# Optimization experiments

Measured on AMD Instinct MI355X. Metric: run time of the kernel, lower is better.

Reference implementation:

```python
import jax, jax.numpy as jnp
import numpy as np

EPS_COS = 1e-8   # torch F.cosine_similarity norm clamp
EPS_LN = 1e-5    # torch LayerNorm eps


def setup_inputs() -> dict:
    key = jax.random.key(0)
    ks = jax.random.split(key, 8)
    B, P, T, D, H = 512, 200000, 4, 64, 256
    return {
        "target_feat": jax.random.normal(ks[0], (B, D), jnp.float32),
        "source_protos": jax.random.normal(ks[1], (P, T, D), jnp.float32),
        "W1": jax.random.normal(ks[2], (3 * D, H), jnp.float32) * 0.05,
        "b1": jnp.zeros((H,), jnp.float32),
        "ln_g": jnp.ones((H,), jnp.float32),
        "ln_b": jnp.zeros((H,), jnp.float32),
        "W2": jax.random.normal(ks[3], (H, H), jnp.float32) * 0.05,
        "b2": jnp.zeros((H,), jnp.float32),
        "W3": jax.random.normal(ks[4], (H, D), jnp.float32) * 0.05,
        "b3": jnp.zeros((D,), jnp.float32),
        "top_k": 3,
    }


def _layernorm(x, g, b):
    mu = jnp.mean(x, axis=-1, keepdims=True)
    var = jnp.mean(jnp.square(x - mu), axis=-1, keepdims=True)
    return (x - mu) * jax.lax.rsqrt(var + EPS_LN) * g + b


def reference(target_feat, source_protos, W1, b1, ln_g, ln_b, W2, b2, W3, b3, top_k):
    # --- retrieve_similar_prototypes (batched over B queries) ---
    centers = jnp.mean(source_protos, axis=1)              # [P, D]
    tn = target_feat / jnp.maximum(
        jnp.linalg.norm(target_feat, axis=-1, keepdims=True), EPS_COS)
    cn = centers / jnp.maximum(
        jnp.linalg.norm(centers, axis=-1, keepdims=True), EPS_COS)
    sims = jnp.einsum("bd,pd->bp", tn, cn)                 # [B, P] cosine sims
    top_vals, top_idx = jax.lax.top_k(sims, top_k)         # [B, K]
    similar_protos = centers[top_idx]                      # [B, K, D] gather

    # --- interpolate_new_prototype ---
    weights = jax.nn.softmax(top_vals, axis=-1)            # [B, K]
    weighted = jnp.einsum("bkd,bk->bd", similar_protos, weights)
    concat = jnp.concatenate(
        [weighted, similar_protos[:, 0], target_feat], axis=-1)  # [B, 3D]

    h = jax.nn.relu(_layernorm(concat @ W1 + b1, ln_g, ln_b))
    h = jax.nn.relu(h @ W2 + b2)
    new_proto = h @ W3 + b3                                # [B, D]
    return new_proto
```

## Files before the change

### kernel.cpp

```cpp
#include <hip/hip_runtime.h>

#define PTOT 200000
#define NB 512
#define DD 64
#define PT 256
#define NBLK ((PTOT + PT - 1) / PT)
#define NPAD (NBLK * PT)
#define NP3 (NBLK * 3)
#define NCAND 8

typedef __attribute__((ext_vector_type(4))) float f32x4;
typedef __attribute__((ext_vector_type(8))) __bf16 bf16x8;

__device__ __forceinline__ ushort f2bf(float f){
  uint u = __float_as_uint(f);
  u += 0x7FFFu + ((u >> 16) & 1u);
  return (ushort)(u >> 16);
}

__device__ __forceinline__ void ins3(uint& k0, uint& k1, uint& k2, uint key){
  uint t0 = k0 > key ? k0 : key;
  uint m0 = k0 > key ? key : k0;
  uint t1 = k1 > m0 ? k1 : m0;
  uint m1 = k1 > m0 ? m0 : k1;
  k2 = k2 > m1 ? k2 : m1;
  k1 = t1; k0 = t0;
}

__global__ __launch_bounds__(256) void kA_stream(const float* __restrict__ sp,
                                                 const float* __restrict__ tf,
                                                 ushort* __restrict__ cn,
                                                 float* __restrict__ tnf,
                                                 ushort* __restrict__ tnb){
  const int gid = blockIdx.x * 256 + threadIdx.x;
  const int row = gid >> 2;
  const int q = gid & 3;
  const bool istgt = row >= NPAD;

  f32x4 v[4][4];
  if (!istgt){
    if (row < PTOT){
      const float* base = sp + (size_t)row * 256 + q * 16;
      #pragma unroll
      for (int t = 0; t < 4; ++t){
        #pragma unroll
        for (int j = 0; j < 4; ++j)
          v[t][j] = *(const f32x4*)(base + t * 64 + j * 4);
      }
    } else {
      #pragma unroll
      for (int t = 0; t < 4; ++t)
        #pragma unroll
        for (int j = 0; j < 4; ++j)
          v[t][j] = (f32x4){0.f, 0.f, 0.f, 0.f};
    }
  } else {
    const float* base = tf + (size_t)(row - NPAD) * 64 + q * 16;
    #pragma unroll
    for (int j = 0; j < 4; ++j){
      v[0][j] = *(const f32x4*)(base + j * 4);
      v[1][j] = v[0][j]; v[2][j] = v[0][j]; v[3][j] = v[0][j];
    }
  }

  f32x4 c[4];
  float ss = 0.f;
  #pragma unroll
  for (int j = 0; j < 4; ++j){
    c[j] = ((v[0][j] + v[1][j]) + (v[2][j] + v[3][j])) * 0.25f;
    ss += c[j].x*c[j].x + c[j].y*c[j].y + c[j].z*c[j].z + c[j].w*c[j].w;
  }
  ss += __shfl_xor(ss, 1, 64);
  ss += __shfl_xor(ss, 2, 64);
  float rn = 1.0f / fmaxf(sqrtf(ss), 1e-8f);

  uint u[8];
  #pragma unroll
  for (int j = 0; j < 4; ++j){
    u[2*j]   = (uint)f2bf(c[j].x * rn) | ((uint)f2bf(c[j].y * rn) << 16);
    u[2*j+1] = (uint)f2bf(c[j].z * rn) | ((uint)f2bf(c[j].w * rn) << 16);
  }
  if (!istgt){
    uint4* dst = (uint4*)(cn + (size_t)row * 64 + q * 16);
    dst[0] = make_uint4(u[0], u[1], u[2], u[3]);
    dst[1] = make_uint4(u[4], u[5], u[6], u[7]);
  } else {
    const int b = row - NPAD;
    float* fd = tnf + (size_t)b * 64 + q * 16;
    #pragma unroll
    for (int j = 0; j < 4; ++j)
      *(f32x4*)(fd + j * 4) = c[j] * rn;
    uint4* hd = (uint4*)(tnb + (size_t)b * 64 + q * 16);
    hd[0] = make_uint4(u[0], u[1], u[2], u[3]);
    hd[1] = make_uint4(u[4], u[5], u[6], u[7]);
  }
}

__global__ __launch_bounds__(256, 4) void kB_scan(const ushort* __restrict__ cn,
                                                  const ushort* __restrict__ tnb,
                                                  uint* __restrict__ cand){
  __shared__ __align__(16) ushort lds[PT * 64];
  const int tid = threadIdx.x;
  const int blk = blockIdx.x;
  const int wave = tid >> 6;
  const int lane = tid & 63;
  const int l15 = lane & 15;
  const int lg  = lane >> 4;

  {
    const char* src = (const char*)(cn + (size_t)blk * PT * 64);
    #pragma unroll
    for (int k = 0; k < 8; ++k){
      int off = (k * 256 + tid) * 16;
      f32x4 v = *(const f32x4*)(src + off);
      int dst = off ^ (((off >> 7) & 7) << 4);
      *(f32x4*)((char*)lds + dst) = v;
    }
  }
  __syncthreads();

  #pragma unroll 2
  for (int bt8 = 0; bt8 < 8; ++bt8){
    const int bt = wave * 8 + bt8;
    const ushort* tp = tnb + (size_t)(bt * 16 + l15) * 64 + lg * 8;
    bf16x8 bf0 = *(const bf16x8*)(tp);
    bf16x8 bf1 = *(const bf16x8*)(tp + 32);
    uint k0 = 0, k1 = 0, k2 = 0;
    #pragma unroll 4
    for (int ps = 0; ps < 16; ++ps){
      const int p = ps * 16 + l15;
      const int base = p * 128;
      const int sw = (p & 7) << 4;
      bf16x8 a0 = *(const bf16x8*)((const char*)lds + ((base + lg * 16) ^ sw));
      bf16x8 a1 = *(const bf16x8*)((const char*)lds + ((base + 64 + lg * 16) ^ sw));
      f32x4 z = {0.f, 0.f, 0.f, 0.f};
      f32x4 acc = __builtin_amdgcn_mfma_f32_16x16x32_bf16(a0, bf0, z, 0, 0, 0);
      acc = __builtin_amdgcn_mfma_f32_16x16x32_bf16(a1, bf1, acc, 0, 0, 0);
      #pragma unroll
      for (int j = 0; j < 4; ++j){
        uint key = (__float_as_uint(fmaxf(acc[j], 0.0f)) & 0xFFFFFE00u)
                 | (uint)(ps * 16 + lg * 4 + j);
        ins3(k0, k1, k2, key);
      }
    }
    #pragma unroll
    for (int m = 16; m <= 32; m <<= 1){
      uint o0 = (uint)__shfl_xor((int)k0, m, 64);
      uint o1 = (uint)__shfl_xor((int)k1, m, 64);
      uint o2 = (uint)__shfl_xor((int)k2, m, 64);
      ins3(k0, k1, k2, o0); ins3(k0, k1, k2, o1); ins3(k0, k1, k2, o2);
    }
    if (lane < 16){
      int b = bt * 16 + l15;
      uint* dst = cand + ((size_t)blk * NB + b) * 3;
      dst[0] = k0; dst[1] = k1; dst[2] = k2;
    }
  }
}

__global__ __launch_bounds__(256) void kC_fuse(const uint* __restrict__ cand,
    const float* __restrict__ sp, const float* __restrict__ tnf,
    const float* __restrict__ tf,
    const float* __restrict__ W1, const float* __restrict__ b1,
    const float* __restrict__ lng, const float* __restrict__ lnb,
    const float* __restrict__ W2, const float* __restrict__ b2,
    const float* __restrict__ W3, const float* __restrict__ b3,
    float* __restrict__ out){
  __shared__ float cc[4][192];
  __shared__ float h1[4][256];
  __shared__ float h2[4][256];
  const int tid = threadIdx.x;
  const int lane = tid & 63;
  const int w = tid >> 6;
  const int rb = blockIdx.x * 4;
  const int b = rb + w;

  uint k0 = 0, k1 = 0, k2 = 0; int j0 = 0, j1 = 0, j2 = 0;
  for (int i = 0; i < (NP3 + 63) / 64; ++i){
    int j = lane + i * 64;
    uint k = 0;
    if (j < NP3){
      int t = j / 3, r = j - t * 3;
      k = cand[(size_t)t * (NB * 3) + b * 3 + r];
    }
    if (k > k0){ k2=k1; j2=j1; k1=k0; j1=j0; k0=k; j0=j; }
    else if (k > k1){ k2=k1; j2=j1; k1=k; j1=j; }
    else if (k > k2){ k2=k; j2=j; }
  }
  int pcand[NCAND];
  #pragma unroll
  for (int it = 0; it < NCAND; ++it){
    uint wk = k0; int wj = j0;
    #pragma unroll
    for (int m = 1; m < 64; m <<= 1){
      uint ok = (uint)__shfl_xor((int)wk, m, 64);
      int  oj = __shfl_xor(wj, m, 64);
      if (ok > wk || (ok == wk && oj > wj)){ wk = ok; wj = oj; }
    }
    pcand[it] = min((wj / 3) * PT + (int)(wk & 0x1FFu), PTOT - 1);
    if (k0 == wk && j0 == wj){ k0=k1; j0=j1; k1=k2; j1=j2; k2=0; j2=0; }
  }
  float xc[NCAND], es[NCAND];
  const float tno = tnf[b * 64 + lane];
  #pragma unroll
  for (int c = 0; c < NCAND; ++c){
    const float* base = sp + (size_t)pcand[c] * 256 + lane;
    float x = 0.25f * (base[0] + base[64] + base[128] + base[192]);
    float ss = x * x;
    float dt = x * tno;
    #pragma unroll
    for (int m = 1; m < 64; m <<= 1){
      ss += __shfl_xor(ss, m, 64);
      dt += __shfl_xor(dt, m, 64);
    }
    xc[c] = x;
    es[c] = dt / fmaxf(sqrtf(ss), 1e-8f);
  }
  float v0 = -3.0e38f, v1 = v0, v2 = v0;
  int s0 = 0, s1 = 0, s2 = 0;
  #pragma unroll
  for (int c = 0; c < NCAND; ++c){
    float v = es[c];
    if (v > v0){ v2=v1; s2=s1; v1=v0; s1=s0; v0=v; s0=c; }
    else if (v > v1){ v2=v1; s2=s1; v1=v; s1=c; }
    else if (v > v2){ v2=v; s2=c; }
  }
  float e1 = expf(v1 - v0), e2 = expf(v2 - v0);
  float inv = 1.0f / (1.0f + e1 + e2);
  float w0 = inv, w1 = e1 * inv, w2 = e2 * inv;
  float wsum = 0.f, ctop = 0.f;
  #pragma unroll
  for (int c = 0; c < NCAND; ++c){
    float coef = (c == s0) ? w0 : (c == s1) ? w1 : (c == s2) ? w2 : 0.f;
    wsum = fmaf(xc[c], coef, wsum);
    ctop += (c == s0) ? xc[c] : 0.f;
  }
  cc[w][lane]       = wsum;
  cc[w][64 + lane]  = ctop;
  cc[w][128 + lane] = tf[b * 64 + lane];
  __syncthreads();

  {
    const int h = tid;
    float a0 = b1[h]; float a1 = a0, a2 = a0, a3 = a0;
    for (int k = 0; k < 192; ++k){
      float wv = W1[k * 256 + h];
      a0 = fmaf(cc[0][k], wv, a0);
      a1 = fmaf(cc[1][k], wv, a1);
      a2 = fmaf(cc[2][k], wv, a2);
      a3 = fmaf(cc[3][k], wv, a3);
    }
    h1[0][h] = a0; h1[1][h] = a1; h1[2][h] = a2; h1[3][h] = a3;
  }
  __syncthreads();
  {
    float v[4]; float s = 0.f, q = 0.f;
    #pragma unroll
    for (int j = 0; j < 4; ++j){
      v[j] = h1[w][lane + 64 * j];
      s += v[j]; q += v[j] * v[j];
    }
    #pragma unroll
    for (int m = 1; m < 64; m <<= 1){
      s += __shfl_xor(s, m, 64);
      q += __shfl_xor(q, m, 64);
    }
    float mu = s * (1.0f / 256.0f);
    float var = q * (1.0f / 256.0f) - mu * mu;
    float rs = rsqrtf(var + 1e-5f);
    #pragma unroll
    for (int j = 0; j < 4; ++j){
      int hh = lane + 64 * j;
      float y = (v[j] - mu) * rs * lng[hh] + lnb[hh];
      h1[w][hh] = fmaxf(y, 0.0f);
    }
  }
  __syncthreads();
  {
    const int h = tid;
    float a0 = b2[h]; float a1 = a0, a2 = a0, a3 = a0;
    for (int k = 0; k < 256; ++k){
      float wv = W2[k * 256 + h];
      a0 = fmaf(h1[0][k], wv, a0);
      a1 = fmaf(h1[1][k], wv, a1);
      a2 = fmaf(h1[2][k], wv, a2);
      a3 = fmaf(h1[3][k], wv, a3);
    }
    h2[0][h] = fmaxf(a0, 0.f); h2[1][h] = fmaxf(a1, 0.f);
    h2[2][h] = fmaxf(a2, 0.f); h2[3][h] = fmaxf(a3, 0.f);
  }
  __syncthreads();
  {
    const int d = tid & 63, q = tid >> 6;
    float a = b3[d];
    for (int k = 0; k < 256; ++k)
      a = fmaf(h2[q][k], W3[k * 64 + d], a);
    out[(size_t)(rb + q) * 64 + d] = a;
  }
}

extern "C" void kernel_launch(void* const* d_in, const int* in_sizes, int n_in,
                              void* d_out, int out_size, void* d_ws, size_t ws_size,
                              hipStream_t stream){
  const float* tf = (const float*)d_in[0];
  const float* sp = (const float*)d_in[1];
  const float* W1 = (const float*)d_in[2];
  const float* b1 = (const float*)d_in[3];
  const float* lng = (const float*)d_in[4];
  const float* lnb = (const float*)d_in[5];
  const float* W2 = (const float*)d_in[6];
  const float* b2 = (const float*)d_in[7];
  const float* W3 = (const float*)d_in[8];
  const float* b3 = (const float*)d_in[9];
  float* out = (float*)d_out;

  char* ws = (char*)d_ws;
  const size_t off_tnb  = 0;
  const size_t off_tnf  = 65536;
  const size_t off_cn   = 65536 + 131072;
  const size_t cn_bytes = (size_t)NPAD * 64 * 2;
  const size_t off_cand = off_cn + cn_bytes;
  const size_t need = off_cand + (size_t)NBLK * NB * 3 * 4;
  if (ws_size < need) return;

  ushort* tnb = (ushort*)(ws + off_tnb);
  float*  tnf = (float*)(ws + off_tnf);
  ushort* cnb = (ushort*)(ws + off_cn);
  uint*   cand = (uint*)(ws + off_cand);

  const int nthreads = (NPAD + NB) * 4;
  kA_stream<<<nthreads / 256, 256, 0, stream>>>(sp, tf, cnb, tnf, tnb);
  kB_scan<<<NBLK, 256, 0, stream>>>(cnb, tnb, cand);
  kC_fuse<<<NB / 4, 256, 0, stream>>>(cand, sp, tnf, tf,
                                      W1, b1, lng, lnb, W2, b2, W3, b3, out);
}
```

Baseline: 132.4 us.

## Fuse prototype center normalization into scan kernel, dropping bf16 intermediate buffer

The center-mean, L2-normalize and bf16 conversion of source prototypes now happen inside the scan kernel, which writes the swizzled bf16 rows straight into LDS instead of staging them through a global buffer. Target normalization moves to a small separate kernel. This removes a global write and re-read of about 25 MB of bf16 centers and one kernel boundary. In exchange, each scan block does more arithmetic and global loads before its first MFMA, which may reduce overlap at the occupancy limit set by launch_bounds(256,4).

```diff
diff --git a/kernel.cpp b/kernel.cpp
--- a/kernel.cpp
+++ b/kernel.cpp
@@ -5,7 +5,6 @@
 #define DD 64
 #define PT 256
 #define NBLK ((PTOT + PT - 1) / PT)
-#define NPAD (NBLK * PT)
 #define NP3 (NBLK * 3)
 #define NCAND 8
 
@@ -27,26 +26,45 @@
   k1 = t1; k0 = t0;
 }
 
-__global__ __launch_bounds__(256) void kA_stream(const float* __restrict__ sp,
-                                                 const float* __restrict__ tf,
-                                                 ushort* __restrict__ cn,
-                                                 float* __restrict__ tnf,
-                                                 ushort* __restrict__ tnb){
-  const int gid = blockIdx.x * 256 + threadIdx.x;
-  const int row = gid >> 2;
-  const int q = gid & 3;
-  const bool istgt = row >= NPAD;
-
-  f32x4 v[4][4];
-  if (!istgt){
-    if (row < PTOT){
-      const float* base = sp + (size_t)row * 256 + q * 16;
+__global__ __launch_bounds__(64) void kT_tn(const float* __restrict__ tf,
+                                            float* __restrict__ tnf,
+                                            ushort* __restrict__ tnb){
+  int b = blockIdx.x, d = threadIdx.x;
+  float v = tf[b * DD + d];
+  float ss = v * v;
+  #pragma unroll
+  for (int m = 1; m < 64; m <<= 1) ss += __shfl_xor(ss, m, 64);
+  float rn = 1.0f / fmaxf(sqrtf(ss), 1e-8f);
+  float t = v * rn;
+  tnf[b * DD + d] = t;
+  tnb[b * DD + d] = f2bf(t);
+}
+
+__global__ __launch_bounds__(256, 4) void kS_scan(const float* __restrict__ sp,
+                                                  const ushort* __restrict__ tnb,
+                                                  uint* __restrict__ cand){
+  __shared__ __align__(16) ushort lds[PT * 64];
+  const int tid = threadIdx.x;
+  const int blk = blockIdx.x;
+  const int q  = tid & 3;
+  const int pr = tid >> 2;
+  const int wave = tid >> 6;
+  const int lane = tid & 63;
+  const int l15 = lane & 15;
+  const int lg  = lane >> 4;
+
+  #pragma unroll
+  for (int pass = 0; pass < 4; ++pass){
+    const int pl = pass * 64 + pr;
+    const int g = blk * PT + pl;
+    f32x4 v[4][4];
+    if (g < PTOT){
+      const float* base = sp + (size_t)g * 256 + q * 16;
       #pragma unroll
-      for (int t = 0; t < 4; ++t){
+      for (int t = 0; t < 4; ++t)
         #pragma unroll
         for (int j = 0; j < 4; ++j)
           v[t][j] = *(const f32x4*)(base + t * 64 + j * 4);
-      }
     } else {
       #pragma unroll
       for (int t = 0; t < 4; ++t)
@@ -54,68 +72,26 @@
         for (int j = 0; j < 4; ++j)
           v[t][j] = (f32x4){0.f, 0.f, 0.f, 0.f};
     }
-  } else {
-    const float* base = tf + (size_t)(row - NPAD) * 64 + q * 16;
+    f32x4 c[4];
+    float ss = 0.f;
     #pragma unroll
     for (int j = 0; j < 4; ++j){
-      v[0][j] = *(const f32x4*)(base + j * 4);
-      v[1][j] = v[0][j]; v[2][j] = v[0][j]; v[3][j] = v[0][j];
-    }
-  }
-
-  f32x4 c[4];
-  float ss = 0.f;
-  #pragma unroll
-  for (int j = 0; j < 4; ++j){
-    c[j] = ((v[0][j] + v[1][j]) + (v[2][j] + v[3][j])) * 0.25f;
-    ss += c[j].x*c[j].x + c[j].y*c[j].y + c[j].z*c[j].z + c[j].w*c[j].w;
-  }
-  ss += __shfl_xor(ss, 1, 64);
-  ss += __shfl_xor(ss, 2, 64);
-  float rn = 1.0f / fmaxf(sqrtf(ss), 1e-8f);
-
-  uint u[8];
-  #pragma unroll
-  for (int j = 0; j < 4; ++j){
-    u[2*j]   = (uint)f2bf(c[j].x * rn) | ((uint)f2bf(c[j].y * rn) << 16);
-    u[2*j+1] = (uint)f2bf(c[j].z * rn) | ((uint)f2bf(c[j].w * rn) << 16);
-  }
-  if (!istgt){
-    uint4* dst = (uint4*)(cn + (size_t)row * 64 + q * 16);
-    dst[0] = make_uint4(u[0], u[1], u[2], u[3]);
-    dst[1] = make_uint4(u[4], u[5], u[6], u[7]);
-  } else {
-    const int b = row - NPAD;
-    float* fd = tnf + (size_t)b * 64 + q * 16;
-    #pragma unroll
-    for (int j = 0; j < 4; ++j)
-      *(f32x4*)(fd + j * 4) = c[j] * rn;
-    uint4* hd = (uint4*)(tnb + (size_t)b * 64 + q * 16);
-    hd[0] = make_uint4(u[0], u[1], u[2], u[3]);
-    hd[1] = make_uint4(u[4], u[5], u[6], u[7]);
-  }
-}
-
-__global__ __launch_bounds__(256, 4) void kB_scan(const ushort* __restrict__ cn,
-                                                  const ushort* __restrict__ tnb,
-                                                  uint* __restrict__ cand){
-  __shared__ __align__(16) ushort lds[PT * 64];
-  const int tid = threadIdx.x;
-  const int blk = blockIdx.x;
-  const int wave = tid >> 6;
-  const int lane = tid & 63;
-  const int l15 = lane & 15;
-  const int lg  = lane >> 4;
-
-  {
-    const char* src = (const char*)(cn + (size_t)blk * PT * 64);
-    #pragma unroll
-    for (int k = 0; k < 8; ++k){
-      int off = (k * 256 + tid) * 16;
-      f32x4 v = *(const f32x4*)(src + off);
-      int dst = off ^ (((off >> 7) & 7) << 4);
-      *(f32x4*)((char*)lds + dst) = v;
-    }
+      c[j] = ((v[0][j] + v[1][j]) + (v[2][j] + v[3][j])) * 0.25f;
+      ss += c[j].x*c[j].x + c[j].y*c[j].y + c[j].z*c[j].z + c[j].w*c[j].w;
+    }
+    ss += __shfl_xor(ss, 1, 64);
+    ss += __shfl_xor(ss, 2, 64);
+    float rn = 1.0f / fmaxf(sqrtf(ss), 1e-8f);
+    uint u[8];
+    #pragma unroll
+    for (int j = 0; j < 4; ++j){
+      u[2*j]   = (uint)f2bf(c[j].x * rn) | ((uint)f2bf(c[j].y * rn) << 16);
+      u[2*j+1] = (uint)f2bf(c[j].z * rn) | ((uint)f2bf(c[j].w * rn) << 16);
+    }
+    const int rowb = pl * 128 + q * 32;
+    const int sw = (pl & 7) << 4;
+    *(uint4*)((char*)lds + ((rowb)      ^ sw)) = make_uint4(u[0], u[1], u[2], u[3]);
+    *(uint4*)((char*)lds + ((rowb + 16) ^ sw)) = make_uint4(u[4], u[5], u[6], u[7]);
   }
   __syncthreads();
 
@@ -317,20 +293,16 @@
   char* ws = (char*)d_ws;
   const size_t off_tnb  = 0;
   const size_t off_tnf  = 65536;
-  const size_t off_cn   = 65536 + 131072;
-  const size_t cn_bytes = (size_t)NPAD * 64 * 2;
-  const size_t off_cand = off_cn + cn_bytes;
+  const size_t off_cand = 65536 + 131072;
   const size_t need = off_cand + (size_t)NBLK * NB * 3 * 4;
   if (ws_size < need) return;
 
   ushort* tnb = (ushort*)(ws + off_tnb);
   float*  tnf = (float*)(ws + off_tnf);
-  ushort* cnb = (ushort*)(ws + off_cn);
   uint*   cand = (uint*)(ws + off_cand);
 
-  const int nthreads = (NPAD + NB) * 4;
-  kA_stream<<<nthreads / 256, 256, 0, stream>>>(sp, tf, cnb, tnf, tnb);
-  kB_scan<<<NBLK, 256, 0, stream>>>(cnb, tnb, cand);
+  kT_tn<<<NB, 64, 0, stream>>>(tf, tnf, tnb);
+  kS_scan<<<NBLK, 256, 0, stream>>>(sp, tnb, cand);
   kC_fuse<<<NB / 4, 256, 0, stream>>>(cand, sp, tnf, tf,
                                       W1, b1, lng, lnb, W2, b2, W3, b3, out);
 }
```

Result: faster. 123.4 us (-6.8%).
